# Performance work log

Hardware: AMD Instinct MI355X
Metric: run time of the kernel (lower is better)

## Reference

```python
import jax, jax.numpy as jnp
import numpy as np

B, H, L, T, D = 2, 12, 1024, 1024, 64
FEA = 3
DIM = H * D  # 768


def setup_inputs() -> dict:
    key = jax.random.key(0)
    ks = jax.random.split(key, 8)
    return {
        "s0": jax.random.normal(ks[0], (B, H, L, T), jnp.float32),
        "s1": jax.random.normal(ks[1], (B, H, L, T), jnp.float32),
        "s2": jax.random.normal(ks[2], (B, H, L, T), jnp.float32),
        "v": jax.random.normal(ks[3], (B, H, T, D), jnp.float32),
        "fuse_w": jax.random.normal(ks[4], (H, H * FEA), jnp.float32) * 0.1,
        "fuse_b": jax.random.normal(ks[5], (H,), jnp.float32) * 0.1,
        "proj_w": jax.random.normal(ks[6], (DIM, DIM), jnp.float32) * 0.02,
        "proj_b": jax.random.normal(ks[7], (DIM,), jnp.float32) * 0.02,
    }


def reference(s0, s1, s2, v, fuse_w, fuse_b, proj_w, proj_b):
    # concat score maps along channel dim: [b, h*fea, l, t]
    scores = jnp.concatenate([s0, s1, s2], axis=1)
    # 1x1 conv fusion over channel dim: [b, h, l, t]
    fused = jnp.einsum('bclt,oc->bolt', scores, fuse_w) + fuse_b[None, :, None, None]
    # softmax over keys (last dim)
    attn = jax.nn.softmax(fused, axis=-1)
    # attn @ V: [b, h, l, d]
    x = jnp.einsum('bhlt,bhtd->bhld', attn, v)
    # merge heads: [b, l, h*d]
    b, h, l, d = x.shape
    x = jnp.transpose(x, (0, 2, 1, 3)).reshape(b, l, h * d)
    # output projection (torch Linear: x @ W.T + b)
    return x @ proj_w.T + proj_b
```

## Files before the change

kernel.cpp:

```cpp
#include <hip/hip_runtime.h>
#include <hip/hip_bf16.h>

typedef __attribute__((ext_vector_type(8))) short short8;
typedef __attribute__((ext_vector_type(8))) unsigned short ushort8;
typedef __attribute__((ext_vector_type(4))) unsigned short u16x4;
typedef __attribute__((ext_vector_type(4))) float f32x4;

#define NB 2
#define NH 12
#define NL 1024
#define NT 1024
#define ND 64
#define NCH 36
#define DIM 768

static __device__ __forceinline__ unsigned short f2bf(float x) {
  union { float f; unsigned int u; } c; c.f = x;
  unsigned int r = c.u + 0x7fffu + ((c.u >> 16) & 1u);
  return (unsigned short)(r >> 16);
}

__global__ __launch_bounds__(256) void k_fuse_softmax(
    const float* __restrict__ s0, const float* __restrict__ s1,
    const float* __restrict__ s2, const float* __restrict__ wT,
    unsigned short* __restrict__ attn)
{
  __shared__ float red[2][4][NH];
  const int tid = threadIdx.x;
  const int b = blockIdx.x >> 10;
  const int l = blockIdx.x & 1023;
  const int wv = tid >> 6, lane = tid & 63;

  float acc[NH][4];
#pragma unroll
  for (int h = 0; h < NH; ++h) {
    acc[h][0] = 0.f; acc[h][1] = 0.f; acc[h][2] = 0.f; acc[h][3] = 0.f;
  }

  const int t0 = tid * 4;
  const size_t base = (size_t)b * NH * NL * NT + (size_t)l * NT + t0;
  const float* ps[3] = { s0 + base, s1 + base, s2 + base };
#pragma unroll
  for (int g = 0; g < 3; ++g) {
    const float* p = ps[g];
#pragma unroll
    for (int ch = 0; ch < NH; ++ch) {
      float4 sv = *(const float4*)(p + (size_t)ch * NL * NT);
      const float* wp = wT + (g * NH + ch) * NH;
#pragma unroll
      for (int h = 0; h < NH; ++h) {
        const float w = wp[h];
        acc[h][0] = fmaf(w, sv.x, acc[h][0]);
        acc[h][1] = fmaf(w, sv.y, acc[h][1]);
        acc[h][2] = fmaf(w, sv.z, acc[h][2]);
        acc[h][3] = fmaf(w, sv.w, acc[h][3]);
      }
    }
  }

  float mx[NH];
#pragma unroll
  for (int h = 0; h < NH; ++h) {
    mx[h] = fmaxf(fmaxf(acc[h][0], acc[h][1]), fmaxf(acc[h][2], acc[h][3]));
#pragma unroll
    for (int off = 32; off > 0; off >>= 1)
      mx[h] = fmaxf(mx[h], __shfl_xor(mx[h], off));
  }
  if (lane == 0) {
#pragma unroll
    for (int h = 0; h < NH; ++h) red[0][wv][h] = mx[h];
  }
  __syncthreads();
#pragma unroll
  for (int h = 0; h < NH; ++h)
    mx[h] = fmaxf(fmaxf(red[0][0][h], red[0][1][h]),
                  fmaxf(red[0][2][h], red[0][3][h]));

  float sm[NH];
#pragma unroll
  for (int h = 0; h < NH; ++h) {
    acc[h][0] = __expf(acc[h][0] - mx[h]);
    acc[h][1] = __expf(acc[h][1] - mx[h]);
    acc[h][2] = __expf(acc[h][2] - mx[h]);
    acc[h][3] = __expf(acc[h][3] - mx[h]);
    sm[h] = (acc[h][0] + acc[h][1]) + (acc[h][2] + acc[h][3]);
#pragma unroll
    for (int off = 32; off > 0; off >>= 1)
      sm[h] += __shfl_xor(sm[h], off);
  }
  if (lane == 0) {
#pragma unroll
    for (int h = 0; h < NH; ++h) red[1][wv][h] = sm[h];
  }
  __syncthreads();

#pragma unroll
  for (int h = 0; h < NH; ++h) {
    float s = (red[1][0][h] + red[1][1][h]) + (red[1][2][h] + red[1][3][h]);
    float inv = 1.0f / s;
    u16x4 u;
    u[0] = f2bf(acc[h][0] * inv);
    u[1] = f2bf(acc[h][1] * inv);
    u[2] = f2bf(acc[h][2] * inv);
    u[3] = f2bf(acc[h][3] * inv);
    *(u16x4*)(attn + ((size_t)(b * NH + h) * NL + l) * NT + t0) = u;
  }
}

__global__ __launch_bounds__(256) void k_transpose_v(
    const float* __restrict__ v, const float* __restrict__ fw,
    unsigned short* __restrict__ vT, float* __restrict__ wT)
{
  __shared__ float vS[128][65];
  const int tid = threadIdx.x;
  const int tt = blockIdx.x;
  const int h = blockIdx.y, b = blockIdx.z;
  if (tt == 0 && h == 0 && b == 0) {
    for (int i = tid; i < NCH * NH; i += 256) {
      int c = i / NH, hh = i % NH;
      wT[c * NH + hh] = fw[hh * NCH + c];
    }
  }
  const int t0 = tt * 128;
  const float* vp = v + ((size_t)(b * NH + h) * NT + t0) * ND;
#pragma unroll
  for (int r = 0; r < 8; ++r) {
    int f = tid + r * 256;
    int t = f >> 4, d4 = (f & 15) * 4;
    float4 x = *(const float4*)(vp + (size_t)t * ND + d4);
    vS[t][d4 + 0] = x.x; vS[t][d4 + 1] = x.y;
    vS[t][d4 + 2] = x.z; vS[t][d4 + 3] = x.w;
  }
  __syncthreads();
  unsigned short* op = vT + (size_t)(b * NH + h) * ND * NT;
#pragma unroll
  for (int r = 0; r < 4; ++r) {
    int c = tid + r * 256;
    int d = c >> 4, tl = (c & 15) * 8;
    ushort8 u;
#pragma unroll
    for (int j = 0; j < 8; ++j) u[j] = f2bf(vS[tl + j][d]);
    *(ushort8*)(op + (size_t)d * NT + t0 + tl) = u;
  }
}

__global__ __launch_bounds__(128) void k_pv(
    const unsigned short* __restrict__ attn,
    const unsigned short* __restrict__ vT,
    unsigned short* __restrict__ xb)
{
  __shared__ unsigned short vS[64][136];
  const int tid = threadIdx.x;
  const int lane = tid & 63, wv = tid >> 6;
  const int lt = blockIdx.x, h = blockIdx.y, b = blockIdx.z;
  const int l0 = lt * 32;
  const unsigned short* ap = attn + ((size_t)(b * NH + h) * NL + l0) * NT;
  const unsigned short* vp = vT + (size_t)(b * NH + h) * ND * NT;
  f32x4 acc[4] = {};
  const int arow = wv * 16 + (lane & 15);
  const int kg = (lane >> 4) * 8;
  const int bn = lane & 15;

  for (int kt = 0; kt < 8; ++kt) {
    __syncthreads();
#pragma unroll
    for (int r = 0; r < 8; ++r) {
      int c = tid + r * 128;
      int d = c >> 4, tl = (c & 15) * 8;
      *(ushort8*)&vS[d][tl] = *(const ushort8*)(vp + (size_t)d * NT + kt * 128 + tl);
    }
    __syncthreads();
#pragma unroll
    for (int ks = 0; ks < 4; ++ks) {
      short8 af = *(const short8*)(ap + (size_t)arow * NT + kt * 128 + ks * 32 + kg);
#pragma unroll
      for (int dt = 0; dt < 4; ++dt) {
        short8 bf = *(const short8*)&vS[dt * 16 + bn][ks * 32 + kg];
        acc[dt] = __builtin_amdgcn_mfma_f32_16x16x32_bf16(af, bf, acc[dt], 0, 0, 0);
      }
    }
  }
  const int crow0 = wv * 16 + (lane >> 4) * 4;
#pragma unroll
  for (int dt = 0; dt < 4; ++dt) {
#pragma unroll
    for (int r = 0; r < 4; ++r) {
      int row = l0 + crow0 + r;
      xb[((size_t)b * NL + row) * DIM + h * ND + dt * 16 + bn] = f2bf(acc[dt][r]);
    }
  }
}

__global__ __launch_bounds__(256) void k_proj(
    const unsigned short* __restrict__ xb, const float* __restrict__ pw,
    const float* __restrict__ pb, float* __restrict__ out)
{
  __shared__ unsigned short wS[64][136];
  const int tid = threadIdx.x;
  const int lane = tid & 63, wv = tid >> 6;
  const int n0 = blockIdx.x * 64, o0 = blockIdx.y * 64;
  f32x4 acc[4] = {};
  const int kg = (lane >> 4) * 8;
  const int bn = lane & 15;
  const int arow = n0 + wv * 16 + bn;

  for (int kt = 0; kt < 6; ++kt) {
    __syncthreads();
#pragma unroll
    for (int r = 0; r < 4; ++r) {
      int c = tid + r * 256;
      int oi = c >> 4, kl = (c & 15) * 8;
      const float* wp = pw + (size_t)(o0 + oi) * DIM + kt * 128 + kl;
      float4 x0 = *(const float4*)(wp);
      float4 x1 = *(const float4*)(wp + 4);
      ushort8 u;
      u[0] = f2bf(x0.x); u[1] = f2bf(x0.y); u[2] = f2bf(x0.z); u[3] = f2bf(x0.w);
      u[4] = f2bf(x1.x); u[5] = f2bf(x1.y); u[6] = f2bf(x1.z); u[7] = f2bf(x1.w);
      *(ushort8*)&wS[oi][kl] = u;
    }
    __syncthreads();
#pragma unroll
    for (int ks = 0; ks < 4; ++ks) {
      short8 af = *(const short8*)(xb + (size_t)arow * DIM + kt * 128 + ks * 32 + kg);
#pragma unroll
      for (int ot = 0; ot < 4; ++ot) {
        short8 bf = *(const short8*)&wS[ot * 16 + bn][ks * 32 + kg];
        acc[ot] = __builtin_amdgcn_mfma_f32_16x16x32_bf16(af, bf, acc[ot], 0, 0, 0);
      }
    }
  }
  const int crow0 = wv * 16 + (lane >> 4) * 4;
#pragma unroll
  for (int ot = 0; ot < 4; ++ot) {
    const int oc = o0 + ot * 16 + bn;
    const float bias = pb[oc];
#pragma unroll
    for (int r = 0; r < 4; ++r) {
      int row = n0 + crow0 + r;
      out[(size_t)row * DIM + oc] = acc[ot][r] + bias;
    }
  }
}

extern "C" void kernel_launch(void* const* d_in, const int* in_sizes, int n_in,
                              void* d_out, int out_size, void* d_ws, size_t ws_size,
                              hipStream_t stream) {
  const float* s0 = (const float*)d_in[0];
  const float* s1 = (const float*)d_in[1];
  const float* s2 = (const float*)d_in[2];
  const float* v  = (const float*)d_in[3];
  const float* fw = (const float*)d_in[4];
  const float* pw = (const float*)d_in[6];
  const float* pb = (const float*)d_in[7];
  float* out = (float*)d_out;

  const size_t attn_bytes = (size_t)NB * NH * NL * NT * 2;
  const size_t vT_bytes   = (size_t)NB * NH * ND * NT * 2;
  const size_t xb_bytes   = (size_t)NB * NL * DIM * 2;
  unsigned short* attn = (unsigned short*)d_ws;
  unsigned short* vT   = (unsigned short*)((char*)d_ws + attn_bytes);
  unsigned short* xb   = (unsigned short*)((char*)d_ws + attn_bytes + vT_bytes);
  float*          wT   = (float*)((char*)d_ws + attn_bytes + vT_bytes + xb_bytes);

  k_transpose_v<<<dim3(8, NH, NB), dim3(256), 0, stream>>>(v, fw, vT, wT);
  k_fuse_softmax<<<dim3(NB * NL), dim3(256), 0, stream>>>(s0, s1, s2, wT, attn);
  k_pv<<<dim3(32, NH, NB), dim3(128), 0, stream>>>(attn, vT, xb);
  k_proj<<<dim3(32, DIM / 64), dim3(256), 0, stream>>>(xb, pw, pb, out);
}
```

Baseline: 115.1 us.

## Stream score maps into LDS with double-buffered direct global-to-LDS loads

The fuse-softmax kernel used to load all 36 channel float4 values straight into registers. It now issues 16-byte global_load_lds transfers in groups of four channels into a double-buffered LDS tile. Explicit vmcnt waits overlap the next group's loads with the current group's FMAs. The goal is to lower register pressure and keep memory traffic flowing steadily. In exchange, each block now uses 32KB of LDS, which may limit occupancy, and fewer loads are in flight per thread than when everything was unrolled. The reduction scratch space now reuses the same LDS buffer.

```diff
diff --git a/kernel.cpp b/kernel.cpp
--- a/kernel.cpp
+++ b/kernel.cpp
@@ -20,16 +20,55 @@
   return (unsigned short)(r >> 16);
 }
 
+static __device__ __forceinline__ void gload_lds16(const float* g, float* l) {
+  __builtin_amdgcn_global_load_lds(
+      (const __attribute__((address_space(1))) void*)g,
+      (__attribute__((address_space(3))) void*)l, 16, 0, 0);
+}
+
+#define K1_ISSUE(BT) do {                                                     \
+    gload_lds16(pall[((BT)*4+0)/12] + (size_t)(((BT)*4+0)%12)*NL*NT + t4,     \
+                &buf[(BT)&1][0][t4]);                                         \
+    gload_lds16(pall[((BT)*4+1)/12] + (size_t)(((BT)*4+1)%12)*NL*NT + t4,     \
+                &buf[(BT)&1][1][t4]);                                         \
+    gload_lds16(pall[((BT)*4+2)/12] + (size_t)(((BT)*4+2)%12)*NL*NT + t4,     \
+                &buf[(BT)&1][2][t4]);                                         \
+    gload_lds16(pall[((BT)*4+3)/12] + (size_t)(((BT)*4+3)%12)*NL*NT + t4,     \
+                &buf[(BT)&1][3][t4]);                                         \
+  } while (0)
+
+#define K1_WAIT4 do { asm volatile("s_waitcnt vmcnt(4)" ::: "memory");        \
+                      __builtin_amdgcn_sched_barrier(0); } while (0)
+#define K1_WAIT0 do { asm volatile("s_waitcnt vmcnt(0)" ::: "memory");        \
+                      __builtin_amdgcn_sched_barrier(0); } while (0)
+
+#define K1_COMP(BT) do {                                                      \
+    _Pragma("unroll")                                                         \
+    for (int j = 0; j < 4; ++j) {                                             \
+      const float4 sv = *(const float4*)&buf[(BT)&1][j][t4];                  \
+      const float* wp = wT + ((BT)*4 + j) * NH;                               \
+      _Pragma("unroll")                                                       \
+      for (int h = 0; h < NH; ++h) {                                          \
+        const float w = wp[h];                                                \
+        acc[h][0] = fmaf(w, sv.x, acc[h][0]);                                 \
+        acc[h][1] = fmaf(w, sv.y, acc[h][1]);                                 \
+        acc[h][2] = fmaf(w, sv.z, acc[h][2]);                                 \
+        acc[h][3] = fmaf(w, sv.w, acc[h][3]);                                 \
+      }                                                                       \
+    }                                                                         \
+  } while (0)
+
 __global__ __launch_bounds__(256) void k_fuse_softmax(
     const float* __restrict__ s0, const float* __restrict__ s1,
     const float* __restrict__ s2, const float* __restrict__ wT,
     unsigned short* __restrict__ attn)
 {
-  __shared__ float red[2][4][NH];
+  __shared__ float buf[2][4][NT];
   const int tid = threadIdx.x;
   const int b = blockIdx.x >> 10;
   const int l = blockIdx.x & 1023;
   const int wv = tid >> 6, lane = tid & 63;
+  const int t4 = tid * 4;
 
   float acc[NH][4];
 #pragma unroll
@@ -37,26 +76,22 @@
     acc[h][0] = 0.f; acc[h][1] = 0.f; acc[h][2] = 0.f; acc[h][3] = 0.f;
   }
 
-  const int t0 = tid * 4;
-  const size_t base = (size_t)b * NH * NL * NT + (size_t)l * NT + t0;
-  const float* ps[3] = { s0 + base, s1 + base, s2 + base };
-#pragma unroll
-  for (int g = 0; g < 3; ++g) {
-    const float* p = ps[g];
-#pragma unroll
-    for (int ch = 0; ch < NH; ++ch) {
-      float4 sv = *(const float4*)(p + (size_t)ch * NL * NT);
-      const float* wp = wT + (g * NH + ch) * NH;
-#pragma unroll
-      for (int h = 0; h < NH; ++h) {
-        const float w = wp[h];
-        acc[h][0] = fmaf(w, sv.x, acc[h][0]);
-        acc[h][1] = fmaf(w, sv.y, acc[h][1]);
-        acc[h][2] = fmaf(w, sv.z, acc[h][2]);
-        acc[h][3] = fmaf(w, sv.w, acc[h][3]);
-      }
-    }
-  }
+  const size_t base = (size_t)b * NH * NL * NT + (size_t)l * NT;
+  const float* pall[3] = { s0 + base, s1 + base, s2 + base };
+
+  K1_ISSUE(0);
+  K1_ISSUE(1); K1_WAIT4; K1_COMP(0);
+  K1_ISSUE(2); K1_WAIT4; K1_COMP(1);
+  K1_ISSUE(3); K1_WAIT4; K1_COMP(2);
+  K1_ISSUE(4); K1_WAIT4; K1_COMP(3);
+  K1_ISSUE(5); K1_WAIT4; K1_COMP(4);
+  K1_ISSUE(6); K1_WAIT4; K1_COMP(5);
+  K1_ISSUE(7); K1_WAIT4; K1_COMP(6);
+  K1_ISSUE(8); K1_WAIT4; K1_COMP(7);
+  K1_WAIT0;    K1_COMP(8);
+
+  __syncthreads();
+  float* red = &buf[0][0][0];
 
   float mx[NH];
 #pragma unroll
@@ -68,13 +103,13 @@
   }
   if (lane == 0) {
 #pragma unroll
-    for (int h = 0; h < NH; ++h) red[0][wv][h] = mx[h];
+    for (int h = 0; h < NH; ++h) red[wv * NH + h] = mx[h];
   }
   __syncthreads();
 #pragma unroll
   for (int h = 0; h < NH; ++h)
-    mx[h] = fmaxf(fmaxf(red[0][0][h], red[0][1][h]),
-                  fmaxf(red[0][2][h], red[0][3][h]));
+    mx[h] = fmaxf(fmaxf(red[0 * NH + h], red[1 * NH + h]),
+                  fmaxf(red[2 * NH + h], red[3 * NH + h]));
 
   float sm[NH];
 #pragma unroll
@@ -90,20 +125,21 @@
   }
   if (lane == 0) {
 #pragma unroll
-    for (int h = 0; h < NH; ++h) red[1][wv][h] = sm[h];
+    for (int h = 0; h < NH; ++h) red[48 + wv * NH + h] = sm[h];
   }
   __syncthreads();
 
 #pragma unroll
   for (int h = 0; h < NH; ++h) {
-    float s = (red[1][0][h] + red[1][1][h]) + (red[1][2][h] + red[1][3][h]);
+    float s = (red[48 + 0 * NH + h] + red[48 + 1 * NH + h]) +
+              (red[48 + 2 * NH + h] + red[48 + 3 * NH + h]);
     float inv = 1.0f / s;
     u16x4 u;
     u[0] = f2bf(acc[h][0] * inv);
     u[1] = f2bf(acc[h][1] * inv);
     u[2] = f2bf(acc[h][2] * inv);
     u[3] = f2bf(acc[h][3] * inv);
-    *(u16x4*)(attn + ((size_t)(b * NH + h) * NL + l) * NT + t0) = u;
+    *(u16x4*)(attn + ((size_t)(b * NH + h) * NL + l) * NT + t4) = u;
   }
 }
 
```

New measurement: 122.0 us. 6.0% more time.

## Double-buffer score loads into LDS via async global_load_lds in fuse-softmax

Applied to the files above, without the earlier changes.

The fuse+softmax kernel now uses 1024-thread blocks that each process four query rows, one per group of four waves. It streams the 36 score channels through a two-stage LDS double buffer using asynchronous global-to-LDS loads and explicit vmcnt waits. The goal is to overlap the memory-bound score reads with the channel-mixing FMAs and to lower register pressure from holding many float4 loads live. The trade-offs are a larger LDS footprint, which may limit blocks per CU, and fewer outstanding loads per wave than a fully unrolled register version.

```diff
diff --git a/kernel.cpp b/kernel.cpp
--- a/kernel.cpp
+++ b/kernel.cpp
@@ -20,16 +20,24 @@
   return (unsigned short)(r >> 16);
 }
 
-__global__ __launch_bounds__(256) void k_fuse_softmax(
+static __device__ __forceinline__ void gload_lds16(const float* g, float* l) {
+  __builtin_amdgcn_global_load_lds(
+      (const __attribute__((address_space(1))) void*)g,
+      (__attribute__((address_space(3))) void*)l, 16, 0, 0);
+}
+
+__global__ __launch_bounds__(1024) void k_fuse_softmax(
     const float* __restrict__ s0, const float* __restrict__ s1,
     const float* __restrict__ s2, const float* __restrict__ wT,
     unsigned short* __restrict__ attn)
 {
-  __shared__ float red[2][4][NH];
-  const int tid = threadIdx.x;
-  const int b = blockIdx.x >> 10;
-  const int l = blockIdx.x & 1023;
+  __shared__ float buf[2][2][4][NT];
+  const int tid = threadIdx.x;
   const int wv = tid >> 6, lane = tid & 63;
+  const int r = wv >> 2, q = wv & 3;
+  const int b = blockIdx.x >> 8;
+  const int l = ((blockIdx.x & 255) << 2) | r;
+  const int toff = q * 256 + lane * 4;
 
   float acc[NH][4];
 #pragma unroll
@@ -37,16 +45,29 @@
     acc[h][0] = 0.f; acc[h][1] = 0.f; acc[h][2] = 0.f; acc[h][3] = 0.f;
   }
 
-  const int t0 = tid * 4;
-  const size_t base = (size_t)b * NH * NL * NT + (size_t)l * NT + t0;
-  const float* ps[3] = { s0 + base, s1 + base, s2 + base };
-#pragma unroll
-  for (int g = 0; g < 3; ++g) {
-    const float* p = ps[g];
-#pragma unroll
-    for (int ch = 0; ch < NH; ++ch) {
-      float4 sv = *(const float4*)(p + (size_t)ch * NL * NT);
-      const float* wp = wT + (g * NH + ch) * NH;
+  const size_t rowbase = (size_t)b * NH * NL * NT + (size_t)l * NT + toff;
+  const float* pall[3] = { s0 + rowbase, s1 + rowbase, s2 + rowbase };
+
+#define K1_SRC(c) (pall[(c) / 12] + (size_t)((c) % 12) * NL * NT)
+
+  gload_lds16(K1_SRC(0), &buf[0][0][r][toff]);
+  gload_lds16(K1_SRC(1), &buf[0][1][r][toff]);
+
+#pragma unroll
+  for (int bt = 0; bt < 18; ++bt) {
+    if (bt < 17) {
+      gload_lds16(K1_SRC(2 * bt + 2), &buf[(bt + 1) & 1][0][r][toff]);
+      gload_lds16(K1_SRC(2 * bt + 3), &buf[(bt + 1) & 1][1][r][toff]);
+      asm volatile("s_waitcnt vmcnt(2)" ::: "memory");
+    } else {
+      asm volatile("s_waitcnt vmcnt(0)" ::: "memory");
+    }
+    __builtin_amdgcn_sched_barrier(0);
+#pragma unroll
+    for (int j = 0; j < 2; ++j) {
+      const int c = 2 * bt + j;
+      const float4 sv = *(const float4*)&buf[bt & 1][j][r][toff];
+      const float* wp = wT + c * NH;
 #pragma unroll
       for (int h = 0; h < NH; ++h) {
         const float w = wp[h];
@@ -57,6 +78,10 @@
       }
     }
   }
+#undef K1_SRC
+
+  __syncthreads();
+  float* red = &buf[0][0][0][0];
 
   float mx[NH];
 #pragma unroll
@@ -68,13 +93,13 @@
   }
   if (lane == 0) {
 #pragma unroll
-    for (int h = 0; h < NH; ++h) red[0][wv][h] = mx[h];
+    for (int h = 0; h < NH; ++h) red[wv * NH + h] = mx[h];
   }
   __syncthreads();
 #pragma unroll
   for (int h = 0; h < NH; ++h)
-    mx[h] = fmaxf(fmaxf(red[0][0][h], red[0][1][h]),
-                  fmaxf(red[0][2][h], red[0][3][h]));
+    mx[h] = fmaxf(fmaxf(red[(r * 4 + 0) * NH + h], red[(r * 4 + 1) * NH + h]),
+                  fmaxf(red[(r * 4 + 2) * NH + h], red[(r * 4 + 3) * NH + h]));
 
   float sm[NH];
 #pragma unroll
@@ -90,20 +115,21 @@
   }
   if (lane == 0) {
 #pragma unroll
-    for (int h = 0; h < NH; ++h) red[1][wv][h] = sm[h];
-  }
-  __syncthreads();
-
-#pragma unroll
-  for (int h = 0; h < NH; ++h) {
-    float s = (red[1][0][h] + red[1][1][h]) + (red[1][2][h] + red[1][3][h]);
+    for (int h = 0; h < NH; ++h) red[192 + wv * NH + h] = sm[h];
+  }
+  __syncthreads();
+
+#pragma unroll
+  for (int h = 0; h < NH; ++h) {
+    float s = (red[192 + (r * 4 + 0) * NH + h] + red[192 + (r * 4 + 1) * NH + h]) +
+              (red[192 + (r * 4 + 2) * NH + h] + red[192 + (r * 4 + 3) * NH + h]);
     float inv = 1.0f / s;
     u16x4 u;
     u[0] = f2bf(acc[h][0] * inv);
     u[1] = f2bf(acc[h][1] * inv);
     u[2] = f2bf(acc[h][2] * inv);
     u[3] = f2bf(acc[h][3] * inv);
-    *(u16x4*)(attn + ((size_t)(b * NH + h) * NL + l) * NT + t0) = u;
+    *(u16x4*)(attn + ((size_t)(b * NH + h) * NL + l) * NT + toff) = u;
   }
 }
 
@@ -263,7 +289,7 @@
   float*          wT   = (float*)((char*)d_ws + attn_bytes + vT_bytes + xb_bytes);
 
   k_transpose_v<<<dim3(8, NH, NB), dim3(256), 0, stream>>>(v, fw, vT, wT);
-  k_fuse_softmax<<<dim3(NB * NL), dim3(256), 0, stream>>>(s0, s1, s2, wT, attn);
+  k_fuse_softmax<<<dim3(NB * 256), dim3(1024), 0, stream>>>(s0, s1, s2, wT, attn);
   k_pv<<<dim3(32, NH, NB), dim3(128), 0, stream>>>(attn, vT, xb);
   k_proj<<<dim3(32, DIM / 64), dim3(256), 0, stream>>>(xb, pw, pb, out);
 }
```

Result: slower. 121.7 us (+5.8%).
